# Performance work log

Measured on AMD Instinct MI355X. Metric: run time of the kernel, lower is better.

Reference implementation:

```python
import jax, jax.numpy as jnp
import numpy as np
import math

B, S, D, H, L = 2, 1024, 512, 8, 4
HD = D // H
FF = 4 * D
EPS = 1e-7
MAX_NORM = 1.0 - 1e-3

def _beta(a, b):
    return math.exp(math.lgamma(a) + math.lgamma(b) - math.lgamma(a + b))

BETA_D = _beta(D / 2.0, 0.5)
BETA_HD = _beta(HD / 2.0, 0.5)

def _norm(x):
    return jnp.sqrt(jnp.maximum(jnp.sum(x * x, axis=-1, keepdims=True), EPS * EPS))

def project(x):
    n = _norm(x)
    return x * jnp.minimum(1.0, MAX_NORM / n)

def expmap0(v):
    n = _norm(v)
    return jnp.tanh(n) * v / n

def logmap0(x):
    n = _norm(x)
    nc = jnp.clip(n, EPS, MAX_NORM)
    return jnp.arctanh(nc) * x / nc

def mobius_add(x, y):
    x2 = jnp.sum(x * x, -1, keepdims=True)
    y2 = jnp.sum(y * y, -1, keepdims=True)
    xy = jnp.sum(x * y, -1, keepdims=True)
    num = (1 + 2 * xy + y2) * x + (1 - x2) * y
    den = jnp.maximum(1 + 2 * xy + x2 * y2, EPS)
    return project(num / den)

def mobius_scalar_mul(r, x):
    n = jnp.clip(_norm(x), EPS, MAX_NORM)
    return jnp.tanh(r * jnp.arctanh(n)) * x / n

def plinear(x, W, b):
    # PoincareLinear: tangent-space affine map expmap0(logmap0(x) @ W.T + b)
    return expmap0(logmap0(x) @ W.T + b)

def pln(x, w, b):
    t = logmap0(x)
    mu = jnp.mean(t, -1, keepdims=True)
    var = jnp.mean((t - mu) ** 2, -1, keepdims=True)
    return expmap0((t - mu) / jnp.sqrt(var + 1e-5) * w + b)

def pairwise_dist(q, k):  # q,k: [B,H,S,hd] on the ball -> [B,H,S,S]
    # dist(x,y) = arccosh(1 + 2||x-y||^2 / ((1-||x||^2)(1-||y||^2))), c=1
    q2 = jnp.sum(q * q, -1)
    k2 = jnp.sum(k * k, -1)
    qk = jnp.einsum('bhid,bhjd->bhij', q, k)
    d2 = jnp.maximum(q2[..., :, None] + k2[..., None, :] - 2 * qk, 0.0)
    den = jnp.maximum((1 - q2)[..., :, None] * (1 - k2)[..., None, :], EPS)
    return jnp.arccosh(jnp.maximum(1.0 + 2.0 * d2 / den, 1.0 + 1e-7))

def weighted_midpoint(w, v):  # Mobius gyromidpoint, w:[B,H,S,S], v:[B,H,S,hd]
    lam = 2.0 / jnp.maximum(1.0 - jnp.sum(v * v, -1, keepdims=True), EPS)
    num = jnp.einsum('bhij,bhjd->bhid', w, lam * v)
    den = jnp.einsum('bhij,bhj->bhi', w, lam[..., 0] - 1.0)
    mid = num / jnp.maximum(den, EPS)[..., None]
    return project(mobius_scalar_mul(0.5, mid))

def split_heads(p):  # beta-split: [B,S,D] -> [B,H,S,hd] on the ball
    t = logmap0(p)
    t = t.reshape(t.shape[0], t.shape[1], H, HD).transpose(0, 2, 1, 3)
    return expmap0(t * (BETA_HD / BETA_D))

def concat_heads(p):  # beta-concat: [B,H,S,hd] -> [B,S,D] on the ball
    t = logmap0(p) * (BETA_D / BETA_HD)
    t = t.transpose(0, 2, 1, 3).reshape(t.shape[0], t.shape[2], D)
    return expmap0(t)

def attention(x, Wq, bq, Wk, bk, Wv, bv, Wo, bo, tau, gamma, mask):
    qh = split_heads(plinear(x, Wq, bq))
    kh = split_heads(plinear(x, Wk, bk))
    vh = split_heads(plinear(x, Wv, bv))
    scores = tau * (-pairwise_dist(qh, kh)) - gamma
    scores = jnp.where(mask, scores, -1e9)
    w = jax.nn.softmax(scores, axis=-1)
    out = concat_heads(weighted_midpoint(w, vh))
    return plinear(out, Wo, bo)

def ffn(x, W1, b1, W2, b2):
    h = plinear(x, W1, b1)
    h = expmap0(jax.nn.relu(logmap0(h)))
    return plinear(h, W2, b2)

def forward(x, pos_tab, ln1_w, ln1_b, ln2_w, ln2_b, Wq, bq, Wk, bk, Wv, bv, Wo, bo, W1, b1, W2, b2, tau, gamma, Wout, bout):
    seq = x.shape[1]
    x = mobius_add(x, pos_tab[None, :seq])
    mask = jnp.tril(jnp.ones((seq, seq), dtype=bool))
    for l in range(L):
        h = pln(x, ln1_w[l], ln1_b[l])
        h = attention(h, Wq[l], bq[l], Wk[l], bk[l], Wv[l], bv[l], Wo[l], bo[l], tau[l], gamma[l], mask)
        x = mobius_add(x, h)
        h = pln(x, ln2_w[l], ln2_b[l])
        h = ffn(h, W1[l], b1[l], W2[l], b2[l])
        x = mobius_add(x, h)
    return plinear(x, Wout, bout)

def setup_inputs():
    ks = jax.random.split(jax.random.key(0), 10)
    r = lambda i, shp, s: s * jax.random.normal(ks[i], shp, dtype=jnp.float32)
    return {
        'x': expmap0(r(0, (B, S, D), 0.05)),
        'pos_tab': expmap0(r(1, (S, D), 0.02)),
        'ln1_w': 0.1 * jnp.ones((L, D), jnp.float32), 'ln1_b': jnp.zeros((L, D), jnp.float32),
        'ln2_w': 0.1 * jnp.ones((L, D), jnp.float32), 'ln2_b': jnp.zeros((L, D), jnp.float32),
        'Wq': r(2, (L, D, D), 0.02), 'bq': jnp.zeros((L, D), jnp.float32),
        'Wk': r(3, (L, D, D), 0.02), 'bk': jnp.zeros((L, D), jnp.float32),
        'Wv': r(4, (L, D, D), 0.02), 'bv': jnp.zeros((L, D), jnp.float32),
        'Wo': r(5, (L, D, D), 0.02), 'bo': jnp.zeros((L, D), jnp.float32),
        'W1': r(6, (L, FF, D), 0.02), 'b1': jnp.zeros((L, FF), jnp.float32),
        'W2': r(7, (L, D, FF), 0.02), 'b2': jnp.zeros((L, D), jnp.float32),
        'tau': jnp.ones((L,), jnp.float32), 'gamma': jnp.zeros((L,), jnp.float32),
        'Wout': r(8, (D, D), 0.02), 'bout': jnp.zeros((D,), jnp.float32),
    }

def reference(x, pos_tab, ln1_w, ln1_b, ln2_w, ln2_b, Wq, bq, Wk, bk, Wv, bv, Wo, bo, W1, b1, W2, b2, tau, gamma, Wout, bout):
    return forward(x, pos_tab, ln1_w, ln1_b, ln2_w, ln2_b, Wq, bq, Wk, bk, Wv, bv, Wo, bo, W1, b1, W2, b2, tau, gamma, Wout, bout)
```

## Files before the change

### kernel.cpp

```cpp
#include <hip/hip_runtime.h>
#include <cmath>

#define B_ 2
#define S_ 1024
#define D_ 512
#define H_ 8
#define HD_ 64
#define FF_ 2048
#define L_ 4
#define N_ (B_*S_)
#define BHS_ (B_*H_*S_)
#define EPSf 1e-7f
#define EPS2f 1e-14f
#define MAXNf 0.999f
#define KSG_ 8
#define KSF_ 2
#define KSA_ 4

typedef unsigned short u16;
typedef __attribute__((ext_vector_type(8))) short s16x8;
typedef __attribute__((ext_vector_type(8))) unsigned short u16x8;
typedef __attribute__((ext_vector_type(4))) float f32x4;

struct F8 { float v[8]; };

__device__ __forceinline__ F8 ld8(const float* __restrict__ p){
  F8 r; const float4 a = *(const float4*)p; const float4 b = *(const float4*)(p+4);
  r.v[0]=a.x; r.v[1]=a.y; r.v[2]=a.z; r.v[3]=a.w;
  r.v[4]=b.x; r.v[5]=b.y; r.v[6]=b.z; r.v[7]=b.w;
  return r;
}
__device__ __forceinline__ void st8(float* __restrict__ p, const F8& r){
  *(float4*)p     = make_float4(r.v[0],r.v[1],r.v[2],r.v[3]);
  *(float4*)(p+4) = make_float4(r.v[4],r.v[5],r.v[6],r.v[7]);
}
__device__ __forceinline__ float ssq8(const F8& r){
  float s=0.f;
#pragma unroll
  for(int i=0;i<8;i++) s = fmaf(r.v[i], r.v[i], s);
  return s;
}
__device__ __forceinline__ float sum8(const F8& r){
  float s=0.f;
#pragma unroll
  for(int i=0;i<8;i++) s += r.v[i];
  return s;
}
__device__ __forceinline__ float wredsum(float v){
#pragma unroll
  for(int o=1;o<64;o<<=1) v += __shfl_xor(v,o,64);
  return v;
}
__device__ __forceinline__ float g8sum(float v){
#pragma unroll
  for(int o=1;o<8;o<<=1) v += __shfl_xor(v,o,64);
  return v;
}

__device__ __forceinline__ void bfsplit(float x, u16& h, u16& l){
  unsigned u = __float_as_uint(x);
  h = (u16)((u + 0x7FFFu + ((u>>16)&1u))>>16);
  float back = __uint_as_float(((unsigned)h)<<16);
  float r = x - back;
  unsigned u2 = __float_as_uint(r);
  l = (u16)((u2 + 0x7FFFu + ((u2>>16)&1u))>>16);
}
__device__ __forceinline__ void st8bf(u16* __restrict__ hp, u16* __restrict__ lp, const F8& r){
  u16x8 h, l;
#pragma unroll
  for(int i=0;i<8;i++){ u16 hh,ll; bfsplit(r.v[i],hh,ll); h[i]=hh; l[i]=ll; }
  *(u16x8*)hp = h; *(u16x8*)lp = l;
}
__device__ __forceinline__ void cvt8(const float* __restrict__ s,
                                     u16* __restrict__ hp, u16* __restrict__ lp){
  F8 x = ld8(s);
  st8bf(hp, lp, x);
}

__device__ __forceinline__ F8 mobius_add8(const F8& x, const F8& y){
  float x2 = wredsum(ssq8(x));
  float y2 = wredsum(ssq8(y));
  float d = 0.f;
#pragma unroll
  for(int i=0;i<8;i++) d = fmaf(x.v[i], y.v[i], d);
  float xy = wredsum(d);
  float cx  = 1.f + 2.f*xy + y2;
  float cy  = 1.f - x2;
  float den = fmaxf(1.f + 2.f*xy + x2*y2, EPSf);
  F8 z;
#pragma unroll
  for(int i=0;i<8;i++) z.v[i] = (cx*x.v[i] + cy*y.v[i]) / den;
  float s2 = wredsum(ssq8(z));
  float n  = sqrtf(fmaxf(s2, EPS2f));
  float pr = fminf(1.f, MAXNf/n);
#pragma unroll
  for(int i=0;i<8;i++) z.v[i] *= pr;
  return z;
}


__global__ void k_mobius_pos(const float* __restrict__ xin, const float* __restrict__ pos,
                             float* __restrict__ xout){
  const int r = blockIdx.x, lane = threadIdx.x;
  const int s = r % S_;
  const size_t o = (size_t)r*D_ + (lane<<3);
  F8 x = ld8(xin + o);
  F8 y = ld8(pos + (size_t)s*D_ + (lane<<3));
  F8 z = mobius_add8(x, y);
  st8(xout + o, z);
}

__global__ void k_mobius_epi(const float* __restrict__ up, float* __restrict__ x){
  const int r = blockIdx.x, lane = threadIdx.x;
  const size_t o = (size_t)r*D_ + (lane<<3);
  F8 u = ld8(up + o);
  for(int ks=1; ks<KSG_; ks++){
    F8 t = ld8(up + (size_t)ks*N_*D_ + o);
#pragma unroll
    for(int i=0;i<8;i++) u.v[i] += t.v[i];
  }
  float s2 = wredsum(ssq8(u));
  float n  = sqrtf(fmaxf(s2, EPS2f));
  float se = tanhf(n)/n;
#pragma unroll
  for(int i=0;i<8;i++) u.v[i] *= se;
  F8 xv = ld8(x + o);
  F8 z = mobius_add8(xv, u);
  st8(x + o, z);
}

__global__ void k_pln_tan(const float* __restrict__ xin, const float* __restrict__ w,
                          const float* __restrict__ b, u16* __restrict__ th,
                          u16* __restrict__ tl){
  const int r = blockIdx.x, lane = threadIdx.x;
  const size_t o = (size_t)r*D_ + (lane<<3);
  F8 x = ld8(xin + o);
  float s2 = wredsum(ssq8(x));
  float n  = sqrtf(fmaxf(s2, EPS2f));
  float nc = fminf(fmaxf(n, EPSf), MAXNf);
  float a  = atanhf(nc)/nc;
  F8 t;
#pragma unroll
  for(int i=0;i<8;i++) t.v[i] = x.v[i]*a;
  float mu = wredsum(sum8(t)) * (1.f/(float)D_);
#pragma unroll
  for(int i=0;i<8;i++) t.v[i] -= mu;
  float var = wredsum(ssq8(t)) * (1.f/(float)D_);
  float inv = 1.f/sqrtf(var + 1e-5f);
  F8 wv = ld8(w + (lane<<3));
  F8 bv = ld8(b + (lane<<3));
  F8 u;
#pragma unroll
  for(int i=0;i<8;i++) u.v[i] = fmaf(t.v[i]*inv, wv.v[i], bv.v[i]);
  float s2u = wredsum(ssq8(u));
  float nu  = sqrtf(fmaxf(s2u, EPS2f));
  float se  = tanhf(nu)/nu;
#pragma unroll
  for(int i=0;i<8;i++) u.v[i] *= se;
  float s2p = wredsum(ssq8(u));
  float npn = sqrtf(fmaxf(s2p, EPS2f));
  float nc2 = fminf(fmaxf(npn, EPSf), MAXNf);
  float al  = atanhf(nc2)/nc2;
#pragma unroll
  for(int i=0;i<8;i++) u.v[i] *= al;
  st8bf(th + o, tl + o, u);
}

__global__ void k_logmap(const float* __restrict__ in, u16* __restrict__ th,
                         u16* __restrict__ tl){
  const int r = blockIdx.x, lane = threadIdx.x;
  const size_t o = (size_t)r*D_ + (lane<<3);
  F8 x = ld8(in + o);
  float s2 = wredsum(ssq8(x));
  float n  = sqrtf(fmaxf(s2, EPS2f));
  float nc = fminf(fmaxf(n, EPSf), MAXNf);
  float a  = atanhf(nc)/nc;
#pragma unroll
  for(int i=0;i<8;i++) x.v[i] *= a;
  st8bf(th + o, tl + o, x);
}

__global__ void k_split(const float* __restrict__ up, float* __restrict__ vout,
                        float* __restrict__ aux, int mode, float betaS){
  const int r = blockIdx.x, lane = threadIdx.x;
  const int b = r / S_, s = r % S_;
  const size_t o = (size_t)r*D_ + (lane<<3);
  F8 u = ld8(up + o);
  for(int ks=1; ks<KSG_; ks++){
    F8 t = ld8(up + (size_t)ks*N_*D_ + o);
#pragma unroll
    for(int i=0;i<8;i++) u.v[i] += t.v[i];
  }
  float s2u = wredsum(ssq8(u));
  float n   = sqrtf(fmaxf(s2u, EPS2f));
  float se  = tanhf(n)/n;
#pragma unroll
  for(int i=0;i<8;i++) u.v[i] *= se;
  float s2p = wredsum(ssq8(u));
  float np  = sqrtf(fmaxf(s2p, EPS2f));
  float nc  = fminf(fmaxf(np, EPSf), MAXNf);
  float al  = atanhf(nc)/nc * betaS;
#pragma unroll
  for(int i=0;i<8;i++) u.v[i] *= al;
  float s2h = g8sum(ssq8(u));
  float nh  = sqrtf(fmaxf(s2h, EPS2f));
  float sh  = tanhf(nh)/nh;
#pragma unroll
  for(int i=0;i<8;i++) u.v[i] *= sh;
  const int head = lane>>3, d0 = (lane&7)<<3;
  const size_t ho = ((size_t)(b*H_+head)*S_ + s)*HD_ + d0;
  if (mode == 2){
    float v2  = g8sum(ssq8(u));
    float lam = 2.f/fmaxf(1.f - v2, EPSf);
    F8 lv;
#pragma unroll
    for(int i=0;i<8;i++) lv.v[i] = u.v[i]*lam;
    st8(vout + ho, lv);
    if((lane&7)==0) aux[(size_t)(b*H_+head)*S_ + s] = lam - 1.f;
  } else {
    st8(vout + ho, u);
    if(mode == 1){
      float k2 = g8sum(ssq8(u));
      if((lane&7)==0) aux[(size_t)(b*H_+head)*S_ + s] = k2;
    }
  }
}

#define AST 68
__global__ __launch_bounds__(256) void k_attn(
    const float* __restrict__ qh, const float* __restrict__ kh,
    const float* __restrict__ k2a, const float* __restrict__ lamv,
    const float* __restrict__ lm1, const float* __restrict__ taup,
    const float* __restrict__ gamp, float* __restrict__ nump,
    float* __restrict__ denp){
  const int bid = blockIdx.x;
  const int bh  = bid >> 6;
  const int qt  = (bid & 63) >> 2;
  const int ks  = bid & 3;
  if ((ks<<2) > qt) return;
  const int tid  = threadIdx.x;
  const int w    = tid >> 6;
  const int lane = tid & 63;
  const int i    = (qt<<6) + lane;
  const float tau = *taup, gam = *gamp;
  __shared__ float Ks[64*AST];
  __shared__ float Vs[64*AST];
  __shared__ float k2s[64];
  __shared__ float l1s[64];
  __shared__ float dden[4][64];
  const float4* qp = (const float4*)(qh + ((size_t)bh*S_ + i)*HD_);
  float4 q[16];
#pragma unroll
  for(int c=0;c<16;c++) q[c] = qp[c];
  float q2 = 0.f;
#pragma unroll
  for(int c=0;c<16;c++){
    q2 = fmaf(q[c].x,q[c].x,q2); q2 = fmaf(q[c].y,q[c].y,q2);
    q2 = fmaf(q[c].z,q[c].z,q2); q2 = fmaf(q[c].w,q[c].w,q2);
  }
  const float omq = 1.f - q2;
  float4 acc[16];
#pragma unroll
  for(int c=0;c<16;c++) acc[c] = make_float4(0.f,0.f,0.f,0.f);
  float dacc = 0.f;
  const int jmax = i;
  for(int kt=0; kt<4; kt++){
    const int j0 = (ks<<8) + (kt<<6);
    if (j0 > (qt<<6)) break;
    __syncthreads();
    const float4* kp = (const float4*)(kh   + ((size_t)bh*S_ + j0)*HD_);
    const float4* vp = (const float4*)(lamv + ((size_t)bh*S_ + j0)*HD_);
#pragma unroll
    for(int it=0; it<4; it++){
      const int f   = (it<<8) + tid;
      const int row = f >> 4, c4 = f & 15;
      ((float4*)(Ks + row*AST))[c4] = kp[f];
      ((float4*)(Vs + row*AST))[c4] = vp[f];
    }
    if (tid < 64)      k2s[tid]     = k2a[(size_t)bh*S_ + j0 + tid];
    else if (tid <128) l1s[tid-64]  = lm1[(size_t)bh*S_ + j0 + tid - 64];
    __syncthreads();
    for(int jj=0; jj<16; jj++){
      const int j = (w<<4) + jj;
      const float4* kr = (const float4*)(Ks + j*AST);
      float dp[4] = {0.f,0.f,0.f,0.f};
#pragma unroll
      for(int c=0;c<16;c++){
        const float4 k4 = kr[c];
        float d = dp[c&3];
        d = fmaf(q[c].x,k4.x,d); d = fmaf(q[c].y,k4.y,d);
        d = fmaf(q[c].z,k4.z,d); d = fmaf(q[c].w,k4.w,d);
        dp[c&3] = d;
      }
      const float dot  = (dp[0]+dp[1]) + (dp[2]+dp[3]);
      const float k2v  = k2s[j];
      const float d2   = fmaxf(q2 + k2v - 2.f*dot, 0.f);
      const float dn   = fmaxf(omq*(1.f-k2v), EPSf);
      const float z    = fmaxf(1.f + 2.f*d2/dn, 1.f + 1e-7f);
      const float dist = __logf(z + __fsqrt_rn(fmaf(z,z,-1.f)));
      const float wgt  = (j0 + j <= jmax) ? __expf(fmaf(-tau, dist, -gam)) : 0.f;
      dacc = fmaf(wgt, l1s[j], dacc);
      const float4* vr = (const float4*)(Vs + j*AST);
#pragma unroll
      for(int c=0;c<16;c++){
        const float4 v4 = vr[c];
        acc[c].x = fmaf(wgt, v4.x, acc[c].x);
        acc[c].y = fmaf(wgt, v4.y, acc[c].y);
        acc[c].z = fmaf(wgt, v4.z, acc[c].z);
        acc[c].w = fmaf(wgt, v4.w, acc[c].w);
      }
    }
  }
  __syncthreads();
  dden[w][lane] = dacc;
  if (w==1){ float4* p=(float4*)(Ks + lane*AST);
#pragma unroll
    for(int c=0;c<16;c++) p[c]=acc[c]; }
  if (w==3){ float4* p=(float4*)(Vs + lane*AST);
#pragma unroll
    for(int c=0;c<16;c++) p[c]=acc[c]; }
  __syncthreads();
  if (w==0){ const float4* p=(const float4*)(Ks + lane*AST);
#pragma unroll
    for(int c=0;c<16;c++){ float4 t=p[c];
      acc[c].x+=t.x; acc[c].y+=t.y; acc[c].z+=t.z; acc[c].w+=t.w; }
    dacc += dden[1][lane]; }
  if (w==2){ const float4* p=(const float4*)(Vs + lane*AST);
#pragma unroll
    for(int c=0;c<16;c++){ float4 t=p[c];
      acc[c].x+=t.x; acc[c].y+=t.y; acc[c].z+=t.z; acc[c].w+=t.w; }
    dacc += dden[3][lane]; }
  __syncthreads();
  if (w==2){ float4* p=(float4*)(Ks + lane*AST);
#pragma unroll
    for(int c=0;c<16;c++) p[c]=acc[c];
    dden[2][lane] = dacc; }
  __syncthreads();
  if (w==0){
    const float4* p=(const float4*)(Ks + lane*AST);
#pragma unroll
    for(int c=0;c<16;c++){ float4 t=p[c];
      acc[c].x+=t.x; acc[c].y+=t.y; acc[c].z+=t.z; acc[c].w+=t.w; }
    dacc += dden[2][lane];
    float4* np = (float4*)(nump + ((size_t)ks*BHS_ + (size_t)bh*S_ + i)*HD_);
#pragma unroll
    for(int c=0;c<16;c++) np[c] = acc[c];
    denp[(size_t)ks*BHS_ + (size_t)bh*S_ + i] = dacc;
  }
}

__global__ void k_combine(const float* __restrict__ nump, const float* __restrict__ denp,
                          float* __restrict__ pout, float betaC){
  const int r = blockIdx.x, lane = threadIdx.x;
  const int b = r / S_, s = r % S_;
  const int nks  = (s >> 8) + 1;
  const int head = lane >> 3;
  const int d0   = (lane & 7) << 3;
  const size_t hrow = (size_t)(b*H_ + head)*S_ + s;
  F8 num;
#pragma unroll
  for(int i=0;i<8;i++) num.v[i]=0.f;
  float den = 0.f;
  for(int ks=0; ks<nks; ks++){
    F8 t = ld8(nump + ((size_t)ks*BHS_ + hrow)*HD_ + d0);
#pragma unroll
    for(int i=0;i<8;i++) num.v[i] += t.v[i];
    den += denp[(size_t)ks*BHS_ + hrow];
  }
  den = fmaxf(den, EPSf);
  F8 y;
#pragma unroll
  for(int i=0;i<8;i++) y.v[i] = num.v[i]/den;
  float s2 = g8sum(ssq8(y));
  float n  = fminf(fmaxf(sqrtf(fmaxf(s2,EPS2f)), EPSf), MAXNf);
  float ms = tanhf(0.5f*atanhf(n))/n;
#pragma unroll
  for(int i=0;i<8;i++) y.v[i] *= ms;
  float s2y = g8sum(ssq8(y));
  float ny  = sqrtf(fmaxf(s2y, EPS2f));
  float pf  = fminf(1.f, MAXNf/ny);
#pragma unroll
  for(int i=0;i<8;i++) y.v[i] *= pf;
  float s2c = g8sum(ssq8(y));
  float np2 = sqrtf(fmaxf(s2c, EPS2f));
  float ncc = fminf(fmaxf(np2, EPSf), MAXNf);
  float al  = atanhf(ncc)/ncc * betaC;
#pragma unroll
  for(int i=0;i<8;i++) y.v[i] *= al;
  float s2t = wredsum(ssq8(y));
  float nt  = sqrtf(fmaxf(s2t, EPS2f));
  float se  = tanhf(nt)/nt;
#pragma unroll
  for(int i=0;i<8;i++) y.v[i] *= se;
  st8(pout + (size_t)r*D_ + head*HD_ + d0, y);
}

__global__ void k_ffn_mid(const float* __restrict__ u, u16* __restrict__ th,
                          u16* __restrict__ tl){
  const int r = blockIdx.x, lane = threadIdx.x;
  const float* p0 = u + (size_t)r*FF_ + (lane<<5);
  const float* p1 = p0 + (size_t)N_*FF_;
  float4 x[8];
#pragma unroll
  for(int c=0;c<8;c++){
    float4 a = *(const float4*)(p0 + (c<<2));
    float4 b = *(const float4*)(p1 + (c<<2));
    x[c] = make_float4(a.x+b.x, a.y+b.y, a.z+b.z, a.w+b.w);
  }
  float ls;
#define SSQ8x4(out) { out=0.f; _Pragma("unroll") for(int c=0;c<8;c++){ out=fmaf(x[c].x,x[c].x,out); out=fmaf(x[c].y,x[c].y,out); out=fmaf(x[c].z,x[c].z,out); out=fmaf(x[c].w,x[c].w,out);} }
#define SCALE8x4(a) { _Pragma("unroll") for(int c=0;c<8;c++){ x[c].x*=(a); x[c].y*=(a); x[c].z*=(a); x[c].w*=(a);} }
  SSQ8x4(ls);
  float s2 = wredsum(ls);
  float n  = sqrtf(fmaxf(s2, EPS2f));
  SCALE8x4(tanhf(n)/n);
  SSQ8x4(ls); s2 = wredsum(ls);
  n = sqrtf(fmaxf(s2, EPS2f));
  float nc = fminf(fmaxf(n, EPSf), MAXNf);
  SCALE8x4(atanhf(nc)/nc);
#pragma unroll
  for(int c=0;c<8;c++){
    x[c].x=fmaxf(x[c].x,0.f); x[c].y=fmaxf(x[c].y,0.f);
    x[c].z=fmaxf(x[c].z,0.f); x[c].w=fmaxf(x[c].w,0.f);
  }
  SSQ8x4(ls); s2 = wredsum(ls);
  n = sqrtf(fmaxf(s2, EPS2f));
  SCALE8x4(tanhf(n)/n);
  SSQ8x4(ls); s2 = wredsum(ls);
  n = sqrtf(fmaxf(s2, EPS2f));
  nc = fminf(fmaxf(n, EPSf), MAXNf);
  SCALE8x4(atanhf(nc)/nc);
  u16* hp = th + (size_t)r*FF_ + (lane<<5);
  u16* lp = tl + (size_t)r*FF_ + (lane<<5);
#pragma unroll
  for(int cc=0; cc<4; cc++){
    F8 f;
    f.v[0]=x[2*cc].x; f.v[1]=x[2*cc].y; f.v[2]=x[2*cc].z; f.v[3]=x[2*cc].w;
    f.v[4]=x[2*cc+1].x; f.v[5]=x[2*cc+1].y; f.v[6]=x[2*cc+1].z; f.v[7]=x[2*cc+1].w;
    st8bf(hp + (cc<<3), lp + (cc<<3), f);
  }
#undef SSQ8x4
#undef SCALE8x4
}

__global__ void k_final(const float* __restrict__ up, float* __restrict__ out){
  const int r = blockIdx.x, lane = threadIdx.x;
  const size_t o = (size_t)r*D_ + (lane<<3);
  F8 u = ld8(up + o);
  for(int ks=1; ks<KSG_; ks++){
    F8 t = ld8(up + (size_t)ks*N_*D_ + o);
#pragma unroll
    for(int i=0;i<8;i++) u.v[i] += t.v[i];
  }
  float s2 = wredsum(ssq8(u));
  float n  = sqrtf(fmaxf(s2, EPS2f));
  float se = tanhf(n)/n;
#pragma unroll
  for(int i=0;i<8;i++) u.v[i] *= se;
  st8(out + o, u);
}

__global__ void k_cvt6(const float* __restrict__ Wq, const float* __restrict__ Wk,
                       const float* __restrict__ Wv, const float* __restrict__ Wo,
                       const float* __restrict__ W1, const float* __restrict__ W2,
                       u16* __restrict__ wb){
  const int t = blockIdx.y;
  const int n = (t<4) ? (D_*D_) : (FF_*D_);
  const int idx = (int)((blockIdx.x*256 + threadIdx.x)<<3);
  if (idx >= n) return;
  const float* src; u16 *hp, *lp;
  switch(t){
    case 0: src=Wq; hp=wb;          lp=wb+262144;  break;
    case 1: src=Wk; hp=wb+524288;   lp=wb+786432;  break;
    case 2: src=Wv; hp=wb+1048576;  lp=wb+1310720; break;
    case 3: src=Wo; hp=wb+1572864;  lp=wb+1835008; break;
    case 4: src=W1; hp=wb+2097152;  lp=wb+3145728; break;
    default:src=W2; hp=wb+4194304;  lp=wb+5242880; break;
  }
  cvt8(src+idx, hp+idx, lp+idx);
}
__global__ void k_cvt1(const float* __restrict__ src, u16* __restrict__ hp,
                       u16* __restrict__ lp){
  const int idx = (int)((blockIdx.x*256 + threadIdx.x)<<3);
  cvt8(src+idx, hp+idx, lp+idx);
}

#define SAH 0
#define SAL 8192
#define SWH 16384
#define SWL 24576
__device__ __forceinline__ void gll16(const void* g, void* l){
  __builtin_amdgcn_global_load_lds((const __attribute__((address_space(1))) void*)g,
                                   (__attribute__((address_space(3))) void*)l, 16, 0, 0);
}
__global__ __launch_bounds__(256) void k_gemm_mfma(
    const u16* __restrict__ Ah, const u16* __restrict__ Al,
    const u16* __restrict__ Wh, const u16* __restrict__ Wl,
    const float* __restrict__ bias, float* __restrict__ C,
    int K, int M, int kslen){
  __shared__ u16 lds[32768];
  const int tid = threadIdx.x;
  const int wv = tid>>6, lane = tid&63;
  const int wr = wv>>1, wc = wv&1;
  const int lhi = lane>>4, llo = lane&15;
  const int m0 = blockIdx.x<<7;
  const int n0 = blockIdx.y<<7;
  const int ks = blockIdx.z;
  f32x4 acc[4][4];
#pragma unroll
  for(int i=0;i<4;i++)
#pragma unroll
    for(int j=0;j<4;j++) acc[i][j] = (f32x4){0.f,0.f,0.f,0.f};
  const int sr = lane>>3;
  const int g  = (lane&7) ^ sr;
  const int kend = (ks+1)*kslen;
  for(int k0 = ks*kslen; k0 < kend; k0 += 64){
    __syncthreads();
#pragma unroll
    for(int t=0;t<4;t++){
      const int row = wv*32 + t*8 + sr;
      const int lo  = (wv*4+t)*512;
      const size_t ga = (size_t)(n0+row)*K + k0 + g*8;
      const size_t gw = (size_t)(m0+row)*K + k0 + g*8;
      gll16(Ah + ga, &lds[SAH+lo]);
      gll16(Al + ga, &lds[SAL+lo]);
      gll16(Wh + gw, &lds[SWH+lo]);
      gll16(Wl + gw, &lds[SWL+lo]);
    }
    __syncthreads();
#pragma unroll
    for(int kc=0;kc<2;kc++){
      s16x8 ah[4], al4[4], wh4[4], wl4[4];
#pragma unroll
      for(int f=0;f<4;f++){
        const int ra = wr*64 + f*16 + llo;
        const int rw = wc*64 + f*16 + llo;
        const int ca = (kc*4 + lhi) ^ (llo&7);
        ah[f]  = *(const s16x8*)&lds[SAH + ra*64 + ca*8];
        al4[f] = *(const s16x8*)&lds[SAL + ra*64 + ca*8];
        wh4[f] = *(const s16x8*)&lds[SWH + rw*64 + ca*8];
        wl4[f] = *(const s16x8*)&lds[SWL + rw*64 + ca*8];
      }
#pragma unroll
      for(int i=0;i<4;i++)
#pragma unroll
        for(int j=0;j<4;j++){
          acc[i][j] = __builtin_amdgcn_mfma_f32_16x16x32_bf16(ah[i],  wh4[j], acc[i][j], 0,0,0);
          acc[i][j] = __builtin_amdgcn_mfma_f32_16x16x32_bf16(ah[i],  wl4[j], acc[i][j], 0,0,0);
          acc[i][j] = __builtin_amdgcn_mfma_f32_16x16x32_bf16(al4[i], wh4[j], acc[i][j], 0,0,0);
        }
    }
  }
  const size_t cbase = (size_t)ks*(size_t)N_*M;
  float bload[4];
#pragma unroll
  for(int j=0;j<4;j++)
    bload[j] = (ks==0) ? bias[m0 + wc*64 + j*16 + llo] : 0.f;
#pragma unroll
  for(int i=0;i<4;i++)
#pragma unroll
    for(int r=0;r<4;r++){
      const int n = n0 + wr*64 + i*16 + lhi*4 + r;
      float* cp = C + cbase + (size_t)n*M + m0 + wc*64 + llo;
#pragma unroll
      for(int j=0;j<4;j++) cp[j*16] = acc[i][j][r] + bload[j];
    }
}

extern "C" void kernel_launch(void* const* d_in, const int* in_sizes, int n_in,
                              void* d_out, int out_size, void* d_ws, size_t ws_size,
                              hipStream_t stream){
  const float* x_in = (const float*)d_in[0];
  const float* pos  = (const float*)d_in[1];
  const float* ln1w = (const float*)d_in[2];
  const float* ln1b = (const float*)d_in[3];
  const float* ln2w = (const float*)d_in[4];
  const float* ln2b = (const float*)d_in[5];
  const float* Wq   = (const float*)d_in[6];
  const float* bq   = (const float*)d_in[7];
  const float* Wk   = (const float*)d_in[8];
  const float* bk   = (const float*)d_in[9];
  const float* Wv   = (const float*)d_in[10];
  const float* bv   = (const float*)d_in[11];
  const float* Wo   = (const float*)d_in[12];
  const float* bo   = (const float*)d_in[13];
  const float* W1   = (const float*)d_in[14];
  const float* b1   = (const float*)d_in[15];
  const float* W2   = (const float*)d_in[16];
  const float* b2   = (const float*)d_in[17];
  const float* tau  = (const float*)d_in[18];
  const float* gam  = (const float*)d_in[19];
  const float* Wout = (const float*)d_in[20];
  const float* bout = (const float*)d_in[21];

  float* ws = (float*)d_ws;
  float* xb  = ws;
  float* ub  = xb  + (size_t)N_*D_;
  float* qhb = ub  + (size_t)KSG_*N_*D_;
  float* khb = qhb + (size_t)N_*D_;
  float* lvb = khb + (size_t)N_*D_;
  float* k2b = lvb + (size_t)N_*D_;
  float* l1b = k2b + (size_t)BHS_;
  float* dnb = l1b + (size_t)BHS_;
  u16*   tbh = (u16*)(dnb + (size_t)KSA_*BHS_);
  u16*   tbl = tbh + (size_t)N_*FF_;
  u16*   wb  = tbl + (size_t)N_*FF_;
  float* nump = ub;
  float* patt = qhb;

  const double bd  = exp(lgamma(D_/2.0)  + lgamma(0.5) - lgamma(D_/2.0  + 0.5));
  const double bhd = exp(lgamma(HD_/2.0) + lgamma(0.5) - lgamma(HD_/2.0 + 0.5));
  const float betaS = (float)(bhd/bd);
  const float betaC = (float)(bd/bhd);

  const dim3 g512(4, 16, KSG_);
  const dim3 gff1(16, 16, KSF_);
  const dim3 gcv(512, 6);

  k_mobius_pos<<<N_,64,0,stream>>>(x_in, pos, xb);
  for(int l=0; l<L_; l++){
    k_cvt6<<<gcv,256,0,stream>>>(Wq + (size_t)l*D_*D_, Wk + (size_t)l*D_*D_,
                                 Wv + (size_t)l*D_*D_, Wo + (size_t)l*D_*D_,
                                 W1 + (size_t)l*FF_*D_, W2 + (size_t)l*D_*FF_, wb);
    k_pln_tan<<<N_,64,0,stream>>>(xb, ln1w + l*D_, ln1b + l*D_, tbh, tbl);
    k_gemm_mfma<<<g512,256,0,stream>>>(tbh, tbl, wb,          wb+262144,  bq + l*D_, ub, 512, 512, 64);
    k_split<<<N_,64,0,stream>>>(ub, qhb, k2b , 0, betaS);
    k_gemm_mfma<<<g512,256,0,stream>>>(tbh, tbl, wb+524288,   wb+786432,  bk + l*D_, ub, 512, 512, 64);
    k_split<<<N_,64,0,stream>>>(ub, khb, k2b, 1, betaS);
    k_gemm_mfma<<<g512,256,0,stream>>>(tbh, tbl, wb+1048576,  wb+1310720, bv + l*D_, ub, 512, 512, 64);
    k_split<<<N_,64,0,stream>>>(ub, lvb, l1b, 2, betaS);
    k_attn<<<1024,256,0,stream>>>(qhb, khb, k2b, lvb, l1b, tau + l, gam + l, nump, dnb);
    k_combine<<<N_,64,0,stream>>>(nump, dnb, patt, betaC);
    k_logmap<<<N_,64,0,stream>>>(patt, tbh, tbl);
    k_gemm_mfma<<<g512,256,0,stream>>>(tbh, tbl, wb+1572864,  wb+1835008, bo + l*D_, ub, 512, 512, 64);
    k_mobius_epi<<<N_,64,0,stream>>>(ub, xb);
    k_pln_tan<<<N_,64,0,stream>>>(xb, ln2w + l*D_, ln2b + l*D_, tbh, tbl);
    k_gemm_mfma<<<gff1,256,0,stream>>>(tbh, tbl, wb+2097152,  wb+3145728, b1 + l*FF_, ub, 512, 2048, 256);
    k_ffn_mid<<<N_,64,0,stream>>>(ub, tbh, tbl);
    k_gemm_mfma<<<g512,256,0,stream>>>(tbh, tbl, wb+4194304,  wb+5242880, b2 + l*D_, ub, 2048, 512, 256);
    k_mobius_epi<<<N_,64,0,stream>>>(ub, xb);
  }
  k_logmap<<<N_,64,0,stream>>>(xb, tbh, tbl);
  k_cvt1<<<128,256,0,stream>>>(Wout, wb, wb+262144);
  k_gemm_mfma<<<g512,256,0,stream>>>(tbh, tbl, wb, wb+262144, bout, ub, 512, 512, 64);
  k_final<<<N_,64,0,stream>>>(ub, (float*)d_out);
}
```

Before: 1.310 ms.

## Move hyperbolic attention QK and PV products onto bf16x3 MFMA

After: 1.059 ms. -19.2%, faster.

```diff
diff --git a/kernel.cpp b/kernel.cpp
--- a/kernel.cpp
+++ b/kernel.cpp
@@ -19,6 +19,7 @@
 
 typedef unsigned short u16;
 typedef __attribute__((ext_vector_type(8))) short s16x8;
+typedef __attribute__((ext_vector_type(4))) short s16x4;
 typedef __attribute__((ext_vector_type(8))) unsigned short u16x8;
 typedef __attribute__((ext_vector_type(4))) float f32x4;
 
@@ -96,6 +97,11 @@
 #pragma unroll
   for(int i=0;i<8;i++) z.v[i] *= pr;
   return z;
+}
+
+__device__ __forceinline__ void gll16(const void* g, void* l){
+  __builtin_amdgcn_global_load_lds((const __attribute__((address_space(1))) void*)g,
+                                   (__attribute__((address_space(3))) void*)l, 16, 0, 0);
 }
 
 
@@ -180,8 +186,9 @@
   st8bf(th + o, tl + o, x);
 }
 
-__global__ void k_split(const float* __restrict__ up, float* __restrict__ vout,
-                        float* __restrict__ aux, int mode, float betaS){
+__global__ void k_split(const float* __restrict__ up, u16* __restrict__ vh,
+                        u16* __restrict__ vl, float* __restrict__ aux,
+                        int mode, float betaS){
   const int r = blockIdx.x, lane = threadIdx.x;
   const int b = r / S_, s = r % S_;
   const size_t o = (size_t)r*D_ + (lane<<3);
@@ -209,28 +216,32 @@
   for(int i=0;i<8;i++) u.v[i] *= sh;
   const int head = lane>>3, d0 = (lane&7)<<3;
   const size_t ho = ((size_t)(b*H_+head)*S_ + s)*HD_ + d0;
+  const float n2 = g8sum(ssq8(u));
   if (mode == 2){
-    float v2  = g8sum(ssq8(u));
-    float lam = 2.f/fmaxf(1.f - v2, EPSf);
-    F8 lv;
-#pragma unroll
-    for(int i=0;i<8;i++) lv.v[i] = u.v[i]*lam;
-    st8(vout + ho, lv);
+    float lam = 2.f/fmaxf(1.f - n2, EPSf);
+#pragma unroll
+    for(int i=0;i<8;i++) u.v[i] *= lam;
     if((lane&7)==0) aux[(size_t)(b*H_+head)*S_ + s] = lam - 1.f;
   } else {
-    st8(vout + ho, u);
-    if(mode == 1){
-      float k2 = g8sum(ssq8(u));
-      if((lane&7)==0) aux[(size_t)(b*H_+head)*S_ + s] = k2;
-    }
-  }
-}
-
-#define AST 68
+    if((lane&7)==0) aux[(size_t)(b*H_+head)*S_ + s] = n2;
+  }
+  st8bf(vh + ho, vl + ho, u);
+}
+
+#define QH_ 0
+#define QL_ 4096
+#define KH_ 8192
+#define KL_ 12288
+#define VTH_ 16384
+#define VTL_ 20480
+#define PH_ 24576
+#define PL_ 28672
 __global__ __launch_bounds__(256) void k_attn(
-    const float* __restrict__ qh, const float* __restrict__ kh,
-    const float* __restrict__ k2a, const float* __restrict__ lamv,
-    const float* __restrict__ lm1, const float* __restrict__ taup,
+    const u16* __restrict__ qhh, const u16* __restrict__ qhl,
+    const u16* __restrict__ khh, const u16* __restrict__ khl,
+    const u16* __restrict__ lvh, const u16* __restrict__ lvl,
+    const float* __restrict__ q2a, const float* __restrict__ k2a,
+    const float* __restrict__ l1a, const float* __restrict__ taup,
     const float* __restrict__ gamp, float* __restrict__ nump,
     float* __restrict__ denp){
   const int bid = blockIdx.x;
@@ -238,114 +249,163 @@
   const int qt  = (bid & 63) >> 2;
   const int ks  = bid & 3;
   if ((ks<<2) > qt) return;
+  __shared__ u16 SH[32768];
+  __shared__ float k2s[64], l1s[64], q2s[64], dden[4][64];
   const int tid  = threadIdx.x;
   const int w    = tid >> 6;
   const int lane = tid & 63;
-  const int i    = (qt<<6) + lane;
+  const int llo  = lane & 15, lhi = lane >> 4;
   const float tau = *taup, gam = *gamp;
-  __shared__ float Ks[64*AST];
-  __shared__ float Vs[64*AST];
-  __shared__ float k2s[64];
-  __shared__ float l1s[64];
-  __shared__ float dden[4][64];
-  const float4* qp = (const float4*)(qh + ((size_t)bh*S_ + i)*HD_);
-  float4 q[16];
-#pragma unroll
-  for(int c=0;c<16;c++) q[c] = qp[c];
-  float q2 = 0.f;
-#pragma unroll
-  for(int c=0;c<16;c++){
-    q2 = fmaf(q[c].x,q[c].x,q2); q2 = fmaf(q[c].y,q[c].y,q2);
-    q2 = fmaf(q[c].z,q[c].z,q2); q2 = fmaf(q[c].w,q[c].w,q2);
-  }
-  const float omq = 1.f - q2;
-  float4 acc[16];
-#pragma unroll
-  for(int c=0;c<16;c++) acc[c] = make_float4(0.f,0.f,0.f,0.f);
-  float dacc = 0.f;
-  const int jmax = i;
+  const size_t hbase = (size_t)bh * S_;
+  const int srow = tid >> 2;
+  const int sc0  = (tid & 3) << 4;
+  const int sg0  = ((sc0 >> 3)    ) ^ (srow & 7);
+  const int sg1  = ((sc0 >> 3) + 1) ^ (srow & 7);
+  {
+    const size_t qo = (hbase + (size_t)((qt<<6) + srow)) * HD_ + sc0;
+    u16x8 a0 = *(const u16x8*)(qhh + qo), a1 = *(const u16x8*)(qhh + qo + 8);
+    u16x8 b0 = *(const u16x8*)(qhl + qo), b1 = *(const u16x8*)(qhl + qo + 8);
+    *(u16x8*)&SH[QH_ + srow*64 + (sg0<<3)] = a0;
+    *(u16x8*)&SH[QH_ + srow*64 + (sg1<<3)] = a1;
+    *(u16x8*)&SH[QL_ + srow*64 + (sg0<<3)] = b0;
+    *(u16x8*)&SH[QL_ + srow*64 + (sg1<<3)] = b1;
+    if (tid >= 128 && tid < 192) q2s[tid-128] = q2a[hbase + (qt<<6) + tid-128];
+  }
+  f32x4 acc[4];
+#pragma unroll
+  for(int df=0;df<4;df++) acc[df] = (f32x4){0.f,0.f,0.f,0.f};
+  float dacc[4] = {0.f,0.f,0.f,0.f};
   for(int kt=0; kt<4; kt++){
     const int j0 = (ks<<8) + (kt<<6);
     if (j0 > (qt<<6)) break;
     __syncthreads();
-    const float4* kp = (const float4*)(kh   + ((size_t)bh*S_ + j0)*HD_);
-    const float4* vp = (const float4*)(lamv + ((size_t)bh*S_ + j0)*HD_);
-#pragma unroll
-    for(int it=0; it<4; it++){
-      const int f   = (it<<8) + tid;
-      const int row = f >> 4, c4 = f & 15;
-      ((float4*)(Ks + row*AST))[c4] = kp[f];
-      ((float4*)(Vs + row*AST))[c4] = vp[f];
-    }
-    if (tid < 64)      k2s[tid]     = k2a[(size_t)bh*S_ + j0 + tid];
-    else if (tid <128) l1s[tid-64]  = lm1[(size_t)bh*S_ + j0 + tid - 64];
+    const size_t kb = (hbase + j0) * HD_;
+    {
+      const size_t ko = kb + (size_t)srow*HD_ + sc0;
+      u16x8 a0 = *(const u16x8*)(khh + ko), a1 = *(const u16x8*)(khh + ko + 8);
+      u16x8 b0 = *(const u16x8*)(khl + ko), b1 = *(const u16x8*)(khl + ko + 8);
+      *(u16x8*)&SH[KH_ + srow*64 + (sg0<<3)] = a0;
+      *(u16x8*)&SH[KH_ + srow*64 + (sg1<<3)] = a1;
+      *(u16x8*)&SH[KL_ + srow*64 + (sg0<<3)] = b0;
+      *(u16x8*)&SH[KL_ + srow*64 + (sg1<<3)] = b1;
+    }
+    {
+      const int j = tid >> 2, d0 = (tid & 3) << 4;
+      const u16* sh = lvh + kb + (size_t)j*HD_ + d0;
+      const u16* sl = lvl + kb + (size_t)j*HD_ + d0;
+      u16x8 a0 = *(const u16x8*)sh, a1 = *(const u16x8*)(sh+8);
+      u16x8 b0 = *(const u16x8*)sl, b1 = *(const u16x8*)(sl+8);
+      const int jc = j >> 3, jr = j & 7;
+#pragma unroll
+      for(int e=0;e<8;e++){
+        const int d = d0 + e;
+        const int off = d*64 + ((jc ^ (d&7))<<3) + jr;
+        SH[VTH_ + off] = a0[e];
+        SH[VTL_ + off] = b0[e];
+      }
+#pragma unroll
+      for(int e=0;e<8;e++){
+        const int d = d0 + 8 + e;
+        const int off = d*64 + ((jc ^ (d&7))<<3) + jr;
+        SH[VTH_ + off] = a1[e];
+        SH[VTL_ + off] = b1[e];
+      }
+    }
+    if (tid < 64)       k2s[tid]    = k2a[hbase + j0 + tid];
+    else if (tid < 128) l1s[tid-64] = l1a[hbase + j0 + tid-64];
     __syncthreads();
-    for(int jj=0; jj<16; jj++){
-      const int j = (w<<4) + jj;
-      const float4* kr = (const float4*)(Ks + j*AST);
-      float dp[4] = {0.f,0.f,0.f,0.f};
-#pragma unroll
-      for(int c=0;c<16;c++){
-        const float4 k4 = kr[c];
-        float d = dp[c&3];
-        d = fmaf(q[c].x,k4.x,d); d = fmaf(q[c].y,k4.y,d);
-        d = fmaf(q[c].z,k4.z,d); d = fmaf(q[c].w,k4.w,d);
-        dp[c&3] = d;
+    f32x4 sacc[4];
+#pragma unroll
+    for(int nf=0;nf<4;nf++) sacc[nf] = (f32x4){0.f,0.f,0.f,0.f};
+#pragma unroll
+    for(int kc=0;kc<2;kc++){
+      const int arow = (w<<4) + llo;
+      const int ach  = ((kc<<2) + lhi) ^ (llo&7);
+      const s16x8 akh = *(const s16x8*)&SH[KH_ + arow*64 + (ach<<3)];
+      const s16x8 akl = *(const s16x8*)&SH[KL_ + arow*64 + (ach<<3)];
+#pragma unroll
+      for(int nf=0;nf<4;nf++){
+        const int brow = (nf<<4) + llo;
+        const s16x8 bqh = *(const s16x8*)&SH[QH_ + brow*64 + (ach<<3)];
+        const s16x8 bql = *(const s16x8*)&SH[QL_ + brow*64 + (ach<<3)];
+        sacc[nf] = __builtin_amdgcn_mfma_f32_16x16x32_bf16(akh, bqh, sacc[nf], 0,0,0);
+        sacc[nf] = __builtin_amdgcn_mfma_f32_16x16x32_bf16(akl, bqh, sacc[nf], 0,0,0);
+        sacc[nf] = __builtin_amdgcn_mfma_f32_16x16x32_bf16(akh, bql, sacc[nf], 0,0,0);
       }
-      const float dot  = (dp[0]+dp[1]) + (dp[2]+dp[3]);
-      const float k2v  = k2s[j];
-      const float d2   = fmaxf(q2 + k2v - 2.f*dot, 0.f);
-      const float dn   = fmaxf(omq*(1.f-k2v), EPSf);
-      const float z    = fmaxf(1.f + 2.f*d2/dn, 1.f + 1e-7f);
-      const float dist = __logf(z + __fsqrt_rn(fmaf(z,z,-1.f)));
-      const float wgt  = (j0 + j <= jmax) ? __expf(fmaf(-tau, dist, -gam)) : 0.f;
-      dacc = fmaf(wgt, l1s[j], dacc);
-      const float4* vr = (const float4*)(Vs + j*AST);
-#pragma unroll
-      for(int c=0;c<16;c++){
-        const float4 v4 = vr[c];
-        acc[c].x = fmaf(wgt, v4.x, acc[c].x);
-        acc[c].y = fmaf(wgt, v4.y, acc[c].y);
-        acc[c].z = fmaf(wgt, v4.z, acc[c].z);
-        acc[c].w = fmaf(wgt, v4.w, acc[c].w);
+    }
+    float k2v[4], omk[4], l1v[4]; int keyr[4];
+#pragma unroll
+    for(int r=0;r<4;r++){
+      const int kk = (w<<4) + (lhi<<2) + r;
+      k2v[r] = k2s[kk]; omk[r] = 1.f - k2v[r]; l1v[r] = l1s[kk]; keyr[r] = j0 + kk;
+    }
+    const int pgr  = (w<<1) + (lhi>>1);
+    const int poff = (lhi&1) << 2;
+#pragma unroll
+    for(int nf=0;nf<4;nf++){
+      const float q2v = q2s[(nf<<4)+llo];
+      const float omq = 1.f - q2v;
+      const int qi = (qt<<6) + (nf<<4) + llo;
+      float wv[4];
+#pragma unroll
+      for(int r=0;r<4;r++){
+        const float dot = sacc[nf][r];
+        const float d2 = fmaxf(q2v + k2v[r] - 2.f*dot, 0.f);
+        const float dn = fmaxf(omq*omk[r], EPSf);
+        const float z  = fmaxf(1.f + 2.f*d2/dn, 1.f + 1e-7f);
+        const float dist = __logf(z + __fsqrt_rn(fmaf(z,z,-1.f)));
+        wv[r] = (keyr[r] <= qi) ? __expf(fmaf(-tau, dist, -gam)) : 0.f;
       }
+      float dp = (wv[0]*l1v[0] + wv[1]*l1v[1]) + (wv[2]*l1v[2] + wv[3]*l1v[3]);
+      dp += __shfl_xor(dp, 16, 64);
+      dp += __shfl_xor(dp, 32, 64);
+      dacc[nf] += dp;
+      u16 h0,l0,h1,l1,h2,l2,h3,l3;
+      bfsplit(wv[0],h0,l0); bfsplit(wv[1],h1,l1);
+      bfsplit(wv[2],h2,l2); bfsplit(wv[3],h3,l3);
+      const int row = (nf<<4) + llo;
+      const int pp  = pgr ^ (llo&7);
+      *(s16x4*)&SH[PH_ + row*64 + (pp<<3) + poff] =
+          (s16x4){(short)h0,(short)h1,(short)h2,(short)h3};
+      *(s16x4*)&SH[PL_ + row*64 + (pp<<3) + poff] =
+          (s16x4){(short)l0,(short)l1,(short)l2,(short)l3};
+    }
+    __syncthreads();
+#pragma unroll
+    for(int kc2=0;kc2<2;kc2++){
+      const int prow = (w<<4) + llo;
+      const int ach  = ((kc2<<2) + lhi) ^ (llo&7);
+      const s16x8 aph = *(const s16x8*)&SH[PH_ + prow*64 + (ach<<3)];
+      const s16x8 apl = *(const s16x8*)&SH[PL_ + prow*64 + (ach<<3)];
+#pragma unroll
+      for(int df=0;df<4;df++){
+        const int vrow = (df<<4) + llo;
+        const s16x8 bvh = *(const s16x8*)&SH[VTH_ + vrow*64 + (ach<<3)];
+        const s16x8 bvl = *(const s16x8*)&SH[VTL_ + vrow*64 + (ach<<3)];
+        acc[df] = __builtin_amdgcn_mfma_f32_16x16x32_bf16(aph, bvh, acc[df], 0,0,0);
+        acc[df] = __builtin_amdgcn_mfma_f32_16x16x32_bf16(apl, bvh, acc[df], 0,0,0);
+        acc[df] = __builtin_amdgcn_mfma_f32_16x16x32_bf16(aph, bvl, acc[df], 0,0,0);
+      }
     }
   }
   __syncthreads();
-  dden[w][lane] = dacc;
-  if (w==1){ float4* p=(float4*)(Ks + lane*AST);
-#pragma unroll
-    for(int c=0;c<16;c++) p[c]=acc[c]; }
-  if (w==3){ float4* p=(float4*)(Vs + lane*AST);
-#pragma unroll
-    for(int c=0;c<16;c++) p[c]=acc[c]; }
+  if (lhi == 0){
+#pragma unroll
+    for(int nf=0;nf<4;nf++) dden[w][(nf<<4)+llo] = dacc[nf];
+  }
   __syncthreads();
-  if (w==0){ const float4* p=(const float4*)(Ks + lane*AST);
-#pragma unroll
-    for(int c=0;c<16;c++){ float4 t=p[c];
-      acc[c].x+=t.x; acc[c].y+=t.y; acc[c].z+=t.z; acc[c].w+=t.w; }
-    dacc += dden[1][lane]; }
-  if (w==2){ const float4* p=(const float4*)(Vs + lane*AST);
-#pragma unroll
-    for(int c=0;c<16;c++){ float4 t=p[c];
-      acc[c].x+=t.x; acc[c].y+=t.y; acc[c].z+=t.z; acc[c].w+=t.w; }
-    dacc += dden[3][lane]; }
-  __syncthreads();
-  if (w==2){ float4* p=(float4*)(Ks + lane*AST);
-#pragma unroll
-    for(int c=0;c<16;c++) p[c]=acc[c];
-    dden[2][lane] = dacc; }
-  __syncthreads();
-  if (w==0){
-    const float4* p=(const float4*)(Ks + lane*AST);
-#pragma unroll
-    for(int c=0;c<16;c++){ float4 t=p[c];
-      acc[c].x+=t.x; acc[c].y+=t.y; acc[c].z+=t.z; acc[c].w+=t.w; }
-    dacc += dden[2][lane];
-    float4* np = (float4*)(nump + ((size_t)ks*BHS_ + (size_t)bh*S_ + i)*HD_);
-#pragma unroll
-    for(int c=0;c<16;c++) np[c] = acc[c];
-    denp[(size_t)ks*BHS_ + (size_t)bh*S_ + i] = dacc;
+  const size_t nb = ((size_t)ks*BHS_ + hbase + (size_t)(qt<<6))*HD_;
+#pragma unroll
+  for(int df=0;df<4;df++)
+#pragma unroll
+    for(int r=0;r<4;r++){
+      const int q = (w<<4) + (lhi<<2) + r;
+      nump[nb + (size_t)q*HD_ + (df<<4) + llo] = acc[df][r];
+    }
+  if (lhi == 0){
+    const int i = (w<<4) + llo;
+    denp[(size_t)ks*BHS_ + hbase + (qt<<6) + i]
+      = dden[0][i] + dden[1][i] + dden[2][i] + dden[3][i];
   }
 }
 
@@ -489,10 +549,6 @@
 #define SAL 8192
 #define SWH 16384
 #define SWL 24576
-__device__ __forceinline__ void gll16(const void* g, void* l){
-  __builtin_amdgcn_global_load_lds((const __attribute__((address_space(1))) void*)g,
-                                   (__attribute__((address_space(3))) void*)l, 16, 0, 0);
-}
 __global__ __launch_bounds__(256) void k_gemm_mfma(
     const u16* __restrict__ Ah, const u16* __restrict__ Al,
     const u16* __restrict__ Wh, const u16* __restrict__ Wl,
@@ -596,17 +652,21 @@
   float* ws = (float*)d_ws;
   float* xb  = ws;
   float* ub  = xb  + (size_t)N_*D_;
-  float* qhb = ub  + (size_t)KSG_*N_*D_;
-  float* khb = qhb + (size_t)N_*D_;
-  float* lvb = khb + (size_t)N_*D_;
-  float* k2b = lvb + (size_t)N_*D_;
-  float* l1b = k2b + (size_t)BHS_;
-  float* dnb = l1b + (size_t)BHS_;
+  float* q2b = ub  + (size_t)KSG_*N_*D_;
+  float* k2b = q2b + BHS_;
+  float* l1b = k2b + BHS_;
+  float* dnb = l1b + BHS_;
   u16*   tbh = (u16*)(dnb + (size_t)KSA_*BHS_);
   u16*   tbl = tbh + (size_t)N_*FF_;
   u16*   wb  = tbl + (size_t)N_*FF_;
+  u16*   qhh = wb  + 6291456;
+  u16*   qhl = qhh + (size_t)N_*D_;
+  u16*   khh = qhl + (size_t)N_*D_;
+  u16*   khl = khh + (size_t)N_*D_;
+  u16*   lvh = khl + (size_t)N_*D_;
+  u16*   lvl = lvh + (size_t)N_*D_;
   float* nump = ub;
-  float* patt = qhb;
+  float* patt = ub + (size_t)KSA_*BHS_*HD_;
 
   const double bd  = exp(lgamma(D_/2.0)  + lgamma(0.5) - lgamma(D_/2.0  + 0.5));
   const double bhd = exp(lgamma(HD_/2.0) + lgamma(0.5) - lgamma(HD_/2.0 + 0.5));
@@ -624,12 +684,13 @@
                                  W1 + (size_t)l*FF_*D_, W2 + (size_t)l*D_*FF_, wb);
     k_pln_tan<<<N_,64,0,stream>>>(xb, ln1w + l*D_, ln1b + l*D_, tbh, tbl);
     k_gemm_mfma<<<g512,256,0,stream>>>(tbh, tbl, wb,          wb+262144,  bq + l*D_, ub, 512, 512, 64);
-    k_split<<<N_,64,0,stream>>>(ub, qhb, k2b , 0, betaS);
+    k_split<<<N_,64,0,stream>>>(ub, qhh, qhl, q2b, 0, betaS);
     k_gemm_mfma<<<g512,256,0,stream>>>(tbh, tbl, wb+524288,   wb+786432,  bk + l*D_, ub, 512, 512, 64);
-    k_split<<<N_,64,0,stream>>>(ub, khb, k2b, 1, betaS);
+    k_split<<<N_,64,0,stream>>>(ub, khh, khl, k2b, 1, betaS);
     k_gemm_mfma<<<g512,256,0,stream>>>(tbh, tbl, wb+1048576,  wb+1310720, bv + l*D_, ub, 512, 512, 64);
-    k_split<<<N_,64,0,stream>>>(ub, lvb, l1b, 2, betaS);
-    k_attn<<<1024,256,0,stream>>>(qhb, khb, k2b, lvb, l1b, tau + l, gam + l, nump, dnb);
+    k_split<<<N_,64,0,stream>>>(ub, lvh, lvl, l1b, 2, betaS);
+    k_attn<<<1024,256,0,stream>>>(qhh, qhl, khh, khl, lvh, lvl,
+                                  q2b, k2b, l1b, tau + l, gam + l, nump, dnb);
     k_combine<<<N_,64,0,stream>>>(nump, dnb, patt, betaC);
     k_logmap<<<N_,64,0,stream>>>(patt, tbh, tbl);
     k_gemm_mfma<<<g512,256,0,stream>>>(tbh, tbl, wb+1572864,  wb+1835008, bo + l*D_, ub, 512, 512, 64);
```
